# Performance work log

Measured on AMD Instinct MI355X. Metric: run time of the kernel, lower is better.

## Reference

```python
import jax, jax.numpy as jnp
import numpy as np

EMBED = 768
HEADS = 12
HEAD_DIM = EMBED // HEADS
HIDDEN = 4 * EMBED
EPS = 1e-5


def _layernorm(x, g, b):
    mu = jnp.mean(x, axis=-1, keepdims=True)
    var = jnp.var(x, axis=-1, keepdims=True)
    return (x - mu) * jax.lax.rsqrt(var + EPS) * g + b


def setup_inputs() -> dict:
    key = jax.random.key(0)
    ks = jax.random.split(key, 12)
    s_e = 1.0 / np.sqrt(EMBED)
    s_h = 1.0 / np.sqrt(HIDDEN)
    return {
        "x": jax.random.normal(ks[0], (2, 2048, EMBED), dtype=jnp.float32),
        "ln1_g": jnp.ones((EMBED,), jnp.float32),
        "ln1_b": jnp.zeros((EMBED,), jnp.float32),
        "qkv_w": jax.random.uniform(ks[1], (EMBED, 3 * EMBED), jnp.float32, -s_e, s_e),
        "qkv_b": jax.random.uniform(ks[2], (3 * EMBED,), jnp.float32, -s_e, s_e),
        "proj_w": jax.random.uniform(ks[3], (EMBED, EMBED), jnp.float32, -s_e, s_e),
        "proj_b": jax.random.uniform(ks[4], (EMBED,), jnp.float32, -s_e, s_e),
        "ln2_g": jnp.ones((EMBED,), jnp.float32),
        "ln2_b": jnp.zeros((EMBED,), jnp.float32),
        "fc1_w": jax.random.uniform(ks[5], (EMBED, HIDDEN), jnp.float32, -s_e, s_e),
        "fc1_b": jax.random.uniform(ks[6], (HIDDEN,), jnp.float32, -s_e, s_e),
        "fc2_w": jax.random.uniform(ks[7], (HIDDEN, EMBED), jnp.float32, -s_h, s_h),
        "fc2_b": jax.random.uniform(ks[8], (EMBED,), jnp.float32, -s_h, s_h),
    }


def reference(x, ln1_g, ln1_b, qkv_w, qkv_b, proj_w, proj_b,
              ln2_g, ln2_b, fc1_w, fc1_b, fc2_w, fc2_b):
    B, L, C = x.shape
    scale = HEAD_DIM ** -0.5

    # --- attention sublayer (pre-LN) ---
    h = _layernorm(x, ln1_g, ln1_b)
    qkv = h @ qkv_w + qkv_b                       # [B, L, 3C]
    qkv = qkv.reshape(B, L, 3, HEADS, HEAD_DIM)
    q = jnp.transpose(qkv[:, :, 0], (0, 2, 1, 3))  # [B, H, L, D]
    k = jnp.transpose(qkv[:, :, 1], (0, 2, 1, 3))
    v = jnp.transpose(qkv[:, :, 2], (0, 2, 1, 3))
    attn = jnp.einsum('bhqd,bhkd->bhqk', q, k) * scale  # [B, H, L, L]
    attn = jax.nn.softmax(attn, axis=-1)
    out = jnp.einsum('bhqk,bhkd->bhqd', attn, v)  # [B, H, L, D]
    out = jnp.transpose(out, (0, 2, 1, 3)).reshape(B, L, C)
    x = x + (out @ proj_w + proj_b)

    # --- FFN sublayer (pre-LN) ---
    h = _layernorm(x, ln2_g, ln2_b)
    h = jax.nn.gelu(h @ fc1_w + fc1_b, approximate=False)
    x = x + (h @ fc2_w + fc2_b)
    return x
```

## Files before the change

kernel.cpp:

```cpp
#include <hip/hip_runtime.h>
#include <hip/hip_bf16.h>
#include <math.h>

#define EMBED   768
#define NHEADS  12
#define HD      64
#define HIDDEN  3072
#define SEQ     2048
#define BATCH   2
#define ROWS    (BATCH*SEQ)

#define QSCALE  0.1803368801111204f

typedef __bf16 bf16_t;
typedef __attribute__((ext_vector_type(8))) __bf16 bf16x8;
typedef __attribute__((ext_vector_type(4))) float f32x4;

static __device__ __forceinline__ f32x4 mfma16(bf16x8 a, bf16x8 b, f32x4 c) {
  return __builtin_amdgcn_mfma_f32_16x16x32_bf16(a, b, c, 0, 0, 0);
}

#if __has_builtin(__builtin_amdgcn_exp2f)
static __device__ __forceinline__ float fast_exp2(float x) {
  return __builtin_amdgcn_exp2f(x);
}
#else
static __device__ __forceinline__ float fast_exp2(float x) { return exp2f(x); }
#endif

#if __has_builtin(__builtin_amdgcn_rcpf)
static __device__ __forceinline__ float fast_rcp(float x) {
  return __builtin_amdgcn_rcpf(x);
}
#else
static __device__ __forceinline__ float fast_rcp(float x) { return 1.0f / x; }
#endif

typedef __attribute__((address_space(1))) const void gas_void;
typedef __attribute__((address_space(3))) void las_void;
static __device__ __forceinline__ void gll16(const void* g, void* l) {
  __builtin_amdgcn_global_load_lds((gas_void*)g, (las_void*)l, 16, 0, 0);
}

__global__ __launch_bounds__(256) void prep_kernel(
    const float* __restrict__ w0, bf16_t* __restrict__ o0,
    const float* __restrict__ w1, bf16_t* __restrict__ o1,
    const float* __restrict__ w2, bf16_t* __restrict__ o2,
    const float* __restrict__ w3, bf16_t* __restrict__ o3,
    const float* __restrict__ x,  const float* __restrict__ g,
    const float* __restrict__ bt, bf16_t* __restrict__ lnout)
{
  __shared__ float tile[32][33];
  __shared__ float red[8];
  int lin = blockIdx.x;
  if (lin < 6912) {
    const float* in; bf16_t* out; int R, C, bx, by;
    if (lin < 1728)      { in = w0; out = o0; R = 768;  C = 2304; bx = lin % 72; by = lin / 72; }
    else if (lin < 2304) { in = w1; out = o1; R = 768;  C = 768;  lin -= 1728; bx = lin % 24; by = lin / 24; }
    else if (lin < 4608) { in = w2; out = o2; R = 768;  C = 3072; lin -= 2304; bx = lin % 96; by = lin / 96; }
    else                 { in = w3; out = o3; R = 3072; C = 768;  lin -= 4608; bx = lin % 24; by = lin / 24; }
    int c0 = bx * 32, r0 = by * 32;
    int tx = threadIdx.x & 31, ty = threadIdx.x >> 5;
    #pragma unroll
    for (int p = 0; p < 4; ++p) {
      int r = ty + p * 8;
      tile[r][tx] = in[(size_t)(r0 + r) * C + c0 + tx];
    }
    __syncthreads();
    #pragma unroll
    for (int p = 0; p < 4; ++p) {
      int cc = ty + p * 8;
      out[(size_t)(c0 + cc) * R + r0 + tx] = (bf16_t)tile[tx][cc];
    }
    return;
  }
  int row = lin - 6912;
  int tid = threadIdx.x;
  const float* xr = x + (size_t)row * EMBED;
  float v0 = xr[tid], v1 = xr[tid + 256], v2 = xr[tid + 512];
  float s  = v0 + v1 + v2;
  float s2 = v0*v0 + v1*v1 + v2*v2;
  #pragma unroll
  for (int o = 32; o >= 1; o >>= 1) {
    s  += __shfl_xor(s,  o, 64);
    s2 += __shfl_xor(s2, o, 64);
  }
  int wave = tid >> 6, lane = tid & 63;
  if (lane == 0) { red[wave] = s; red[wave + 4] = s2; }
  __syncthreads();
  s  = red[0] + red[1] + red[2] + red[3];
  s2 = red[4] + red[5] + red[6] + red[7];
  float mu  = s * (1.0f / EMBED);
  float var = s2 * (1.0f / EMBED) - mu * mu;
  float rs  = rsqrtf(var + 1e-5f);
  bf16_t* orow = lnout + (size_t)row * EMBED;
  orow[tid]       = (bf16_t)((v0 - mu) * rs * g[tid]       + bt[tid]);
  orow[tid + 256] = (bf16_t)((v1 - mu) * rs * g[tid + 256] + bt[tid + 256]);
  orow[tid + 512] = (bf16_t)((v2 - mu) * rs * g[tid + 512] + bt[tid + 512]);
}

__global__ __launch_bounds__(256) void ln_kernel(
    const float* __restrict__ x, const float* __restrict__ g,
    const float* __restrict__ bt, bf16_t* __restrict__ out)
{
  int row = blockIdx.x;
  int tid = threadIdx.x;
  const float* xr = x + (size_t)row * EMBED;
  float v0 = xr[tid], v1 = xr[tid + 256], v2 = xr[tid + 512];
  float s  = v0 + v1 + v2;
  float s2 = v0*v0 + v1*v1 + v2*v2;
  #pragma unroll
  for (int o = 32; o >= 1; o >>= 1) {
    s  += __shfl_xor(s,  o, 64);
    s2 += __shfl_xor(s2, o, 64);
  }
  __shared__ float red[8];
  int wave = tid >> 6, lane = tid & 63;
  if (lane == 0) { red[wave] = s; red[wave + 4] = s2; }
  __syncthreads();
  s  = red[0] + red[1] + red[2] + red[3];
  s2 = red[4] + red[5] + red[6] + red[7];
  float mu  = s * (1.0f / EMBED);
  float var = s2 * (1.0f / EMBED) - mu * mu;
  float rs  = rsqrtf(var + 1e-5f);
  bf16_t* orow = out + (size_t)row * EMBED;
  orow[tid]       = (bf16_t)((v0 - mu) * rs * g[tid]       + bt[tid]);
  orow[tid + 256] = (bf16_t)((v1 - mu) * rs * g[tid + 256] + bt[tid + 256]);
  orow[tid + 512] = (bf16_t)((v2 - mu) * rs * g[tid + 512] + bt[tid + 512]);
}

template<int MODE, int BN>
__global__ __launch_bounds__(256) void gemm_kernel(
    const bf16_t* __restrict__ A, const bf16_t* __restrict__ WT,
    const float* __restrict__ bias, const float* __restrict__ res,
    void* __restrict__ outp, bf16_t* __restrict__ vt, int N, int K)
{
  constexpr int JT = BN / 32;
  __shared__ bf16_t As[128 * 64];
  __shared__ bf16_t Bs[BN * 64];
  int tid = threadIdx.x;
  int lane = tid & 63, wave = tid >> 6;
  int l15 = lane & 15, quad = lane >> 4;
  int wm = wave >> 1, wn = wave & 1;

  int Nn = N / BN;
  int lin = blockIdx.x;
  int khalf = 0, k_lo = 0, k_hi = K;
  if (MODE == 4) { khalf = lin & 1; lin >>= 1; k_lo = khalf * (K / 2); k_hi = k_lo + K / 2; }
  int bm = (lin & 7) + 8 * ((lin >> 3) / Nn);
  int bn = (lin >> 3) % Nn;
  int m0 = bm * 128, n0 = bn * BN;

  f32x4 acc[4][JT];
  #pragma unroll
  for (int i = 0; i < 4; ++i)
    #pragma unroll
    for (int j = 0; j < JT; ++j)
      acc[i][j] = (f32x4){0.f, 0.f, 0.f, 0.f};

  int grow = lane >> 3;
  int gcol = ((lane & 7) ^ grow) * 8;
  const bf16_t* abase = A  + (size_t)(m0 + wave * 32 + grow) * K + gcol;
  const bf16_t* bbase = WT + (size_t)(n0 + wave * (BN / 4) + grow) * K + gcol;
  int swk = l15 & 7;

  for (int k0 = k_lo; k0 < k_hi; k0 += 64) {
    #pragma unroll
    for (int a = 0; a < 4; ++a)
      gll16(abase + (size_t)a * 8 * K + k0, &As[(wave * 32 + a * 8) * 64]);
    #pragma unroll
    for (int a = 0; a < BN / 32; ++a)
      gll16(bbase + (size_t)a * 8 * K + k0, &Bs[(wave * (BN / 4) + a * 8) * 64]);
    __syncthreads();

    #pragma unroll
    for (int g = 0; g < 2; ++g) {
      bf16x8 af[4], bfr[JT];
      #pragma unroll
      for (int i = 0; i < 4; ++i)
        af[i] = *(const bf16x8*)
            &As[(wm * 64 + i * 16 + l15) * 64 + (((g * 4 + quad) ^ swk) * 8)];
      #pragma unroll
      for (int j = 0; j < JT; ++j)
        bfr[j] = *(const bf16x8*)
            &Bs[(wn * (BN / 2) + j * 16 + l15) * 64 + (((g * 4 + quad) ^ swk) * 8)];
      #pragma unroll
      for (int i = 0; i < 4; ++i)
        #pragma unroll
        for (int j = 0; j < JT; ++j)
          acc[i][j] = mfma16(af[i], bfr[j], acc[i][j]);
    }
    __syncthreads();
  }

  #pragma unroll
  for (int i = 0; i < 4; ++i) {
    int mbase = m0 + wm * 64 + i * 16 + quad * 4;
    #pragma unroll
    for (int j = 0; j < JT; ++j) {
      int n = n0 + wn * (BN / 2) + j * 16 + l15;
      float bn_ = (MODE == 4 && khalf != 0) ? 0.f : bias[n];
      if (MODE == 3 && n >= 1536) {
        int dcol = n - 1536;
        int hh = dcol >> 6, dd = dcol & 63;
        int bsel = mbase >> 11, l = mbase & 2047;
        union { bf16_t b4[4]; uint2 u; } pk;
        #pragma unroll
        for (int r = 0; r < 4; ++r)
          pk.b4[r] = (bf16_t)(acc[i][j][r] + bn_);
        *(uint2*)&vt[(((size_t)bsel * NHEADS + hh) * HD + dd) * SEQ + l] = pk.u;
        continue;
      }
      #pragma unroll
      for (int r = 0; r < 4; ++r) {
        size_t idx = (size_t)(mbase + r) * N + n;
        float v = acc[i][j][r] + bn_;
        if (MODE == 1) {
          float e = fast_exp2(fminf(v * (2.3020807f + 0.10293776f * v * v), 120.f));
          v = v * e * fast_rcp(e + 1.0f);
        }
        if (MODE == 3 && n < 768) v *= QSCALE;
        if (MODE == 2) {
          v += res[idx];
          ((float*)outp)[idx] = v;
        } else if (MODE == 4) {
          atomicAdd((float*)outp + idx, v);
        } else {
          ((bf16_t*)outp)[idx] = (bf16_t)v;
        }
      }
    }
  }
}

__global__ __launch_bounds__(256, 2) void attn_kernel(
    const bf16_t* __restrict__ qkv, const bf16_t* __restrict__ vt,
    bf16_t* __restrict__ attnout)
{
  __attribute__((aligned(16))) __shared__ bf16_t smem[4 * 8192 + 4 * 2 * 640];
  __shared__ float dsumf[4][128];

  int qt = blockIdx.x, h = blockIdx.y, b = blockIdx.z;
  int tid = threadIdx.x;
  int wave = tid >> 6, lane = tid & 63;
  int l15 = lane & 15, quad = lane >> 4;
  int q0 = qt * 128;
  int bh = b * NHEADS + h;

  bf16_t* wbase = smem + wave * 8192;
  bf16_t* pt0   = smem + 32768 + wave * 1280;

  bf16x8 bq[8][2];
  #pragma unroll
  for (int qi = 0; qi < 8; ++qi) {
    const bf16_t* qrow = qkv + (size_t)(b * SEQ + q0 + qi * 16 + l15) * 2304
                             + h * HD + quad * 8;
    bq[qi][0] = *(const bf16x8*)qrow;
    bq[qi][1] = *(const bf16x8*)(qrow + 32);
  }
  __asm__ volatile("s_waitcnt vmcnt(0)" ::: "memory");

  f32x4 accO[8][4];
  #pragma unroll
  for (int qi = 0; qi < 8; ++qi)
    #pragma unroll
    for (int t2 = 0; t2 < 4; ++t2)
      accO[qi][t2] = (f32x4){0.f, 0.f, 0.f, 0.f};
  float lpart[8] = {};

  int krow_l = lane >> 3;
  int kchunk = ((lane & 7) ^ krow_l) * 8;
  const bf16_t* ksrc0 = qkv + (size_t)(b * SEQ + wave * 32 + krow_l) * 2304
                            + 768 + h * HD + kchunk;
  int vrow_l = lane >> 2;
  int vchunk = ((lane & 3) ^ (vrow_l & 3)) * 8;
  const bf16_t* vsrc0 = vt + ((size_t)bh * HD + vrow_l) * SEQ + wave * 32 + vchunk;

  constexpr int NIT = SEQ / 128;

  {
    bf16_t* kb = wbase;
    bf16_t* vb = wbase + 2048;
    #pragma unroll
    for (int p = 0; p < 4; ++p) {
      gll16(ksrc0 + (size_t)(p * 8) * 2304, kb + p * 512);
      gll16(vsrc0 + (size_t)(p * 16) * SEQ, vb + p * 512);
    }
  }

  int cb = 0;
  for (int it = 0; it < NIT; ++it) {
    {
      int kvn = ((it + 1) & (NIT - 1)) * 128;
      const bf16_t* ks = ksrc0 + (size_t)kvn * 2304;
      const bf16_t* vs = vsrc0 + kvn;
      bf16_t* kb = wbase + (cb ^ 1) * 4096;
      bf16_t* vb = kb + 2048;
      #pragma unroll
      for (int p = 0; p < 4; ++p) {
        gll16(ks + (size_t)(p * 8) * 2304, kb + p * 512);
        gll16(vs + (size_t)(p * 16) * SEQ, vb + p * 512);
      }
    }
    __asm__ volatile("s_waitcnt vmcnt(8)" ::: "memory");

    const bf16_t* kb = wbase + cb * 4096;
    const bf16_t* vb = kb + 2048;

    bf16x8 ak[2][2];
    #pragma unroll
    for (int t = 0; t < 2; ++t)
      #pragma unroll
      for (int f = 0; f < 2; ++f)
        ak[t][f] = *(const bf16x8*)
            &kb[(t * 16 + l15) * 64 + (((f * 4 + quad) ^ (l15 & 7)) * 8)];

    bf16x8 bv[4];
    #pragma unroll
    for (int t2 = 0; t2 < 4; ++t2)
      bv[t2] = *(const bf16x8*)
          &vb[(t2 * 16 + l15) * 32 + ((quad ^ (l15 & 3)) * 8)];

    #pragma unroll
    for (int qi = 0; qi < 8; ++qi) {
      bf16_t* pt = pt0 + (qi & 1) * 640;
      #pragma unroll
      for (int t = 0; t < 2; ++t) {
        f32x4 s = (f32x4){0.f, 0.f, 0.f, 0.f};
        s = mfma16(ak[t][0], bq[qi][0], s);
        s = mfma16(ak[t][1], bq[qi][1], s);
        union { bf16_t b4[4]; uint2 u; } pk;
        float ls = 0.f;
        #pragma unroll
        for (int r = 0; r < 4; ++r) {
          float pv = fast_exp2(s[r]);
          ls += pv;
          pk.b4[r] = (bf16_t)pv;
        }
        lpart[qi] += ls;
        *(uint2*)&pt[l15 * 40 + t * 16 + quad * 4] = pk.u;
      }
      bf16x8 ap = *(const bf16x8*)&pt[l15 * 40 + quad * 8];
      #pragma unroll
      for (int t2 = 0; t2 < 4; ++t2)
        accO[qi][t2] = mfma16(ap, bv[t2], accO[qi][t2]);
    }
    cb ^= 1;
  }

  #pragma unroll
  for (int qi = 0; qi < 8; ++qi) {
    float l = lpart[qi];
    l += __shfl_xor(l, 16, 64);
    l += __shfl_xor(l, 32, 64);
    if (quad == 0) dsumf[wave][qi * 16 + l15] = l;
  }
  __syncthreads();

  float* slabf = (float*)smem;
  int rq = lane >> 3;
  int d0 = (lane & 7) * 8;

  for (int pass = 0; pass < 4; ++pass) {
    #pragma unroll
    for (int qi2 = 0; qi2 < 2; ++qi2) {
      int qi = pass * 2 + qi2;
      #pragma unroll
      for (int t2 = 0; t2 < 4; ++t2)
        #pragma unroll
        for (int r = 0; r < 4; ++r)
          slabf[wave * 2048 + (qi2 * 16 + quad * 4 + r) * 64 + t2 * 16 + l15]
              = accO[qi][t2][r];
    }
    __syncthreads();
    int q_loc = wave * 8 + rq;
    f32x4 o0 = (f32x4){0.f,0.f,0.f,0.f}, o1 = (f32x4){0.f,0.f,0.f,0.f};
    #pragma unroll
    for (int sw = 0; sw < 4; ++sw) {
      o0 += *(const f32x4*)&slabf[sw * 2048 + q_loc * 64 + d0];
      o1 += *(const f32x4*)&slabf[sw * 2048 + q_loc * 64 + d0 + 4];
    }
    int q_abs = pass * 32 + q_loc;
    float den = dsumf[0][q_abs] + dsumf[1][q_abs] + dsumf[2][q_abs] + dsumf[3][q_abs];
    float inv = 1.0f / den;
    bf16_t ob[8];
    #pragma unroll
    for (int j = 0; j < 4; ++j) {
      ob[j]     = (bf16_t)(o0[j] * inv);
      ob[j + 4] = (bf16_t)(o1[j] * inv);
    }
    *(uint4*)&attnout[(size_t)(b * SEQ + q0 + q_abs) * EMBED + h * HD + d0]
        = *(const uint4*)ob;
    if (pass < 3) __syncthreads();
  }
}

extern "C" void kernel_launch(void* const* d_in, const int* in_sizes, int n_in,
                              void* d_out, int out_size, void* d_ws, size_t ws_size,
                              hipStream_t stream) {
  (void)in_sizes; (void)n_in; (void)out_size; (void)ws_size;
  const float* x      = (const float*)d_in[0];
  const float* ln1_g  = (const float*)d_in[1];
  const float* ln1_b  = (const float*)d_in[2];
  const float* qkv_w  = (const float*)d_in[3];
  const float* qkv_b  = (const float*)d_in[4];
  const float* proj_w = (const float*)d_in[5];
  const float* proj_b = (const float*)d_in[6];
  const float* ln2_g  = (const float*)d_in[7];
  const float* ln2_b  = (const float*)d_in[8];
  const float* fc1_w  = (const float*)d_in[9];
  const float* fc1_b  = (const float*)d_in[10];
  const float* fc2_w  = (const float*)d_in[11];
  const float* fc2_b  = (const float*)d_in[12];
  float* out = (float*)d_out;

  char* p = (char*)d_ws;
  bf16_t* wqkvT  = (bf16_t*)p; p += (size_t)2304 * 768 * 2;
  bf16_t* wprojT = (bf16_t*)p; p += (size_t)768 * 768 * 2;
  bf16_t* wfc1T  = (bf16_t*)p; p += (size_t)3072 * 768 * 2;
  bf16_t* wfc2T  = (bf16_t*)p; p += (size_t)768 * 3072 * 2;
  bf16_t* hbuf   = (bf16_t*)p; p += (size_t)ROWS * 768 * 2;
  bf16_t* qkv    = (bf16_t*)p;
  bf16_t* hid    = (bf16_t*)p; p += (size_t)ROWS * 3072 * 2;
  bf16_t* vt     = (bf16_t*)p; p += (size_t)BATCH * NHEADS * HD * SEQ * 2;
  bf16_t* attno  = (bf16_t*)p; p += (size_t)ROWS * 768 * 2;

  prep_kernel<<<6912 + ROWS, 256, 0, stream>>>(
      qkv_w, wqkvT, proj_w, wprojT, fc1_w, wfc1T, fc2_w, wfc2T,
      x, ln1_g, ln1_b, hbuf);

  gemm_kernel<3,128><<<32 * (2304/128), 256, 0, stream>>>(
      hbuf, wqkvT, qkv_b, nullptr, qkv, vt, 2304, 768);
  attn_kernel<<<dim3(SEQ/128, NHEADS, BATCH), 256, 0, stream>>>(qkv, vt, attno);
  gemm_kernel<2,64><<<32 * (768/64), 256, 0, stream>>>(
      attno, wprojT, proj_b, x, out, nullptr, 768, 768);

  ln_kernel<<<ROWS, 256, 0, stream>>>(out, ln2_g, ln2_b, hbuf);
  gemm_kernel<1,128><<<32 * (3072/128), 256, 0, stream>>>(
      hbuf, wfc1T, fc1_b, nullptr, hid, nullptr, 3072, 768);
  gemm_kernel<4,64><<<2 * 32 * (768/64), 256, 0, stream>>>(
      hid, wfc2T, fc2_b, nullptr, out, nullptr, 768, 3072);
}
```

Measured before the change: 269.6 us.

## Shrink attention query tile to 64 and feed P to PV MFMA from registers

```diff
diff --git a/kernel.cpp b/kernel.cpp
--- a/kernel.cpp
+++ b/kernel.cpp
@@ -14,13 +14,37 @@
 
 typedef __bf16 bf16_t;
 typedef __attribute__((ext_vector_type(8))) __bf16 bf16x8;
+typedef __attribute__((ext_vector_type(4))) __bf16 bf16x4;
+typedef __attribute__((ext_vector_type(4))) short s16x4;
 typedef __attribute__((ext_vector_type(4))) float f32x4;
 
 static __device__ __forceinline__ f32x4 mfma16(bf16x8 a, bf16x8 b, f32x4 c) {
   return __builtin_amdgcn_mfma_f32_16x16x32_bf16(a, b, c, 0, 0, 0);
 }
 
-#if __has_builtin(__builtin_amdgcn_exp2f)
+static __device__ __forceinline__ f32x4 mfma16x16(bf16x4 a, bf16x4 b, f32x4 c) {
+#if defined(__HIP_DEVICE_COMPILE__)
+# if __has_builtin(__builtin_amdgcn_mfma_f32_16x16x16bf16_1k)
+  s16x4 ai, bi;
+  __builtin_memcpy(&ai, &a, 8);
+  __builtin_memcpy(&bi, &b, 8);
+  return __builtin_amdgcn_mfma_f32_16x16x16bf16_1k(ai, bi, c, 0, 0, 0);
+# elif __has_builtin(__builtin_amdgcn_mfma_f32_16x16x16_bf16)
+  return __builtin_amdgcn_mfma_f32_16x16x16_bf16(a, b, c, 0, 0, 0);
+# else
+  bf16x8 a8 = {a[0], a[1], a[2], a[3],
+               (bf16_t)0.f, (bf16_t)0.f, (bf16_t)0.f, (bf16_t)0.f};
+  bf16x8 b8 = {b[0], b[1], b[2], b[3],
+               (bf16_t)0.f, (bf16_t)0.f, (bf16_t)0.f, (bf16_t)0.f};
+  return mfma16(a8, b8, c);
+# endif
+#else
+  (void)a; (void)b;
+  return c;
+#endif
+}
+
+#if defined(__HIP_DEVICE_COMPILE__) && __has_builtin(__builtin_amdgcn_exp2f)
 static __device__ __forceinline__ float fast_exp2(float x) {
   return __builtin_amdgcn_exp2f(x);
 }
@@ -28,7 +52,7 @@
 static __device__ __forceinline__ float fast_exp2(float x) { return exp2f(x); }
 #endif
 
-#if __has_builtin(__builtin_amdgcn_rcpf)
+#if defined(__HIP_DEVICE_COMPILE__) && __has_builtin(__builtin_amdgcn_rcpf)
 static __device__ __forceinline__ float fast_rcp(float x) {
   return __builtin_amdgcn_rcpf(x);
 }
@@ -233,26 +257,25 @@
   }
 }
 
-__global__ __launch_bounds__(256, 2) void attn_kernel(
+__global__ __launch_bounds__(256, 3) void attn_kernel(
     const bf16_t* __restrict__ qkv, const bf16_t* __restrict__ vt,
     bf16_t* __restrict__ attnout)
 {
-  __attribute__((aligned(16))) __shared__ bf16_t smem[4 * 8192 + 4 * 2 * 640];
-  __shared__ float dsumf[4][128];
+  __attribute__((aligned(16))) __shared__ bf16_t smem[4 * 4096];
+  __shared__ float dsumf[4][64];
 
   int qt = blockIdx.x, h = blockIdx.y, b = blockIdx.z;
   int tid = threadIdx.x;
   int wave = tid >> 6, lane = tid & 63;
   int l15 = lane & 15, quad = lane >> 4;
-  int q0 = qt * 128;
+  int q0 = qt * 64;
   int bh = b * NHEADS + h;
 
-  bf16_t* wbase = smem + wave * 8192;
-  bf16_t* pt0   = smem + 32768 + wave * 1280;
-
-  bf16x8 bq[8][2];
-  #pragma unroll
-  for (int qi = 0; qi < 8; ++qi) {
+  bf16_t* wbase = smem + wave * 4096;
+
+  bf16x8 bq[4][2];
+  #pragma unroll
+  for (int qi = 0; qi < 4; ++qi) {
     const bf16_t* qrow = qkv + (size_t)(b * SEQ + q0 + qi * 16 + l15) * 2304
                              + h * HD + quad * 8;
     bq[qi][0] = *(const bf16x8*)qrow;
@@ -260,96 +283,87 @@
   }
   __asm__ volatile("s_waitcnt vmcnt(0)" ::: "memory");
 
-  f32x4 accO[8][4];
-  #pragma unroll
-  for (int qi = 0; qi < 8; ++qi)
+  f32x4 accO[4][4];
+  #pragma unroll
+  for (int qi = 0; qi < 4; ++qi)
     #pragma unroll
     for (int t2 = 0; t2 < 4; ++t2)
       accO[qi][t2] = (f32x4){0.f, 0.f, 0.f, 0.f};
-  float lpart[8] = {};
+  float lpart[4] = {};
 
   int krow_l = lane >> 3;
   int kchunk = ((lane & 7) ^ krow_l) * 8;
-  const bf16_t* ksrc0 = qkv + (size_t)(b * SEQ + wave * 32 + krow_l) * 2304
+  const bf16_t* ksrc0 = qkv + (size_t)(b * SEQ + wave * 16 + krow_l) * 2304
                             + 768 + h * HD + kchunk;
-  int vrow_l = lane >> 2;
-  int vchunk = ((lane & 3) ^ (vrow_l & 3)) * 8;
-  const bf16_t* vsrc0 = vt + ((size_t)bh * HD + vrow_l) * SEQ + wave * 32 + vchunk;
-
-  constexpr int NIT = SEQ / 128;
+  int vrow_l = lane >> 1;
+  int vchunk = (lane & 1) * 8;
+  const bf16_t* vsrc0 = vt + ((size_t)bh * HD + vrow_l) * SEQ + wave * 16 + vchunk;
+
+  constexpr int NIT = SEQ / 64;
 
   {
     bf16_t* kb = wbase;
-    bf16_t* vb = wbase + 2048;
-    #pragma unroll
-    for (int p = 0; p < 4; ++p) {
+    bf16_t* vb = wbase + 1024;
+    #pragma unroll
+    for (int p = 0; p < 2; ++p) {
       gll16(ksrc0 + (size_t)(p * 8) * 2304, kb + p * 512);
-      gll16(vsrc0 + (size_t)(p * 16) * SEQ, vb + p * 512);
+      gll16(vsrc0 + (size_t)(p * 32) * SEQ, vb + p * 512);
     }
   }
 
   int cb = 0;
   for (int it = 0; it < NIT; ++it) {
     {
-      int kvn = ((it + 1) & (NIT - 1)) * 128;
+      int kvn = ((it + 1) & (NIT - 1)) * 64;
       const bf16_t* ks = ksrc0 + (size_t)kvn * 2304;
       const bf16_t* vs = vsrc0 + kvn;
-      bf16_t* kb = wbase + (cb ^ 1) * 4096;
-      bf16_t* vb = kb + 2048;
-      #pragma unroll
-      for (int p = 0; p < 4; ++p) {
+      bf16_t* kb = wbase + (cb ^ 1) * 2048;
+      bf16_t* vb = kb + 1024;
+      #pragma unroll
+      for (int p = 0; p < 2; ++p) {
         gll16(ks + (size_t)(p * 8) * 2304, kb + p * 512);
-        gll16(vs + (size_t)(p * 16) * SEQ, vb + p * 512);
+        gll16(vs + (size_t)(p * 32) * SEQ, vb + p * 512);
       }
     }
-    __asm__ volatile("s_waitcnt vmcnt(8)" ::: "memory");
-
-    const bf16_t* kb = wbase + cb * 4096;
-    const bf16_t* vb = kb + 2048;
-
-    bf16x8 ak[2][2];
-    #pragma unroll
-    for (int t = 0; t < 2; ++t)
-      #pragma unroll
-      for (int f = 0; f < 2; ++f)
-        ak[t][f] = *(const bf16x8*)
-            &kb[(t * 16 + l15) * 64 + (((f * 4 + quad) ^ (l15 & 7)) * 8)];
-
-    bf16x8 bv[4];
+    __asm__ volatile("s_waitcnt vmcnt(4)" ::: "memory");
+
+    const bf16_t* kb = wbase + cb * 2048;
+    const bf16_t* vb = kb + 1024;
+
+    bf16x8 ak[2];
+    #pragma unroll
+    for (int f = 0; f < 2; ++f)
+      ak[f] = *(const bf16x8*)
+          &kb[l15 * 64 + (((f * 4 + quad) ^ (l15 & 7)) * 8)];
+
+    bf16x4 bv[4];
     #pragma unroll
     for (int t2 = 0; t2 < 4; ++t2)
-      bv[t2] = *(const bf16x8*)
-          &vb[(t2 * 16 + l15) * 32 + ((quad ^ (l15 & 3)) * 8)];
-
-    #pragma unroll
-    for (int qi = 0; qi < 8; ++qi) {
-      bf16_t* pt = pt0 + (qi & 1) * 640;
-      #pragma unroll
-      for (int t = 0; t < 2; ++t) {
-        f32x4 s = (f32x4){0.f, 0.f, 0.f, 0.f};
-        s = mfma16(ak[t][0], bq[qi][0], s);
-        s = mfma16(ak[t][1], bq[qi][1], s);
-        union { bf16_t b4[4]; uint2 u; } pk;
-        float ls = 0.f;
-        #pragma unroll
-        for (int r = 0; r < 4; ++r) {
-          float pv = fast_exp2(s[r]);
-          ls += pv;
-          pk.b4[r] = (bf16_t)pv;
-        }
-        lpart[qi] += ls;
-        *(uint2*)&pt[l15 * 40 + t * 16 + quad * 4] = pk.u;
+      bv[t2] = *(const bf16x4*)&vb[(t2 * 16 + l15) * 16 + quad * 4];
+
+    #pragma unroll
+    for (int qi = 0; qi < 4; ++qi) {
+      f32x4 s = (f32x4){0.f, 0.f, 0.f, 0.f};
+      s = mfma16(ak[0], bq[qi][0], s);
+      s = mfma16(ak[1], bq[qi][1], s);
+      bf16x4 ap;
+      float ls = 0.f;
+      #pragma unroll
+      for (int r = 0; r < 4; ++r) {
+        float pv = fast_exp2(s[r]);
+        ls += pv;
+        ap[r] = (bf16_t)pv;
       }
-      bf16x8 ap = *(const bf16x8*)&pt[l15 * 40 + quad * 8];
+      lpart[qi] += ls;
       #pragma unroll
       for (int t2 = 0; t2 < 4; ++t2)
-        accO[qi][t2] = mfma16(ap, bv[t2], accO[qi][t2]);
+        accO[qi][t2] = mfma16x16(ap, bv[t2], accO[qi][t2]);
     }
     cb ^= 1;
   }
 
   #pragma unroll
-  for (int qi = 0; qi < 8; ++qi) {
+  for (int qi = 0; qi < 4; ++qi) {
     float l = lpart[qi];
     l += __shfl_xor(l, 16, 64);
     l += __shfl_xor(l, 32, 64);
@@ -358,10 +372,8 @@
   __syncthreads();
 
   float* slabf = (float*)smem;
-  int rq = lane >> 3;
-  int d0 = (lane & 7) * 8;
-
-  for (int pass = 0; pass < 4; ++pass) {
+
+  for (int pass = 0; pass < 2; ++pass) {
     #pragma unroll
     for (int qi2 = 0; qi2 < 2; ++qi2) {
       int qi = pass * 2 + qi2;
@@ -373,14 +385,15 @@
               = accO[qi][t2][r];
     }
     __syncthreads();
-    int q_loc = wave * 8 + rq;
+    int row = tid >> 3;
+    int d0 = (tid & 7) * 8;
     f32x4 o0 = (f32x4){0.f,0.f,0.f,0.f}, o1 = (f32x4){0.f,0.f,0.f,0.f};
     #pragma unroll
     for (int sw = 0; sw < 4; ++sw) {
-      o0 += *(const f32x4*)&slabf[sw * 2048 + q_loc * 64 + d0];
-      o1 += *(const f32x4*)&slabf[sw * 2048 + q_loc * 64 + d0 + 4];
-    }
-    int q_abs = pass * 32 + q_loc;
+      o0 += *(const f32x4*)&slabf[sw * 2048 + row * 64 + d0];
+      o1 += *(const f32x4*)&slabf[sw * 2048 + row * 64 + d0 + 4];
+    }
+    int q_abs = pass * 32 + row;
     float den = dsumf[0][q_abs] + dsumf[1][q_abs] + dsumf[2][q_abs] + dsumf[3][q_abs];
     float inv = 1.0f / den;
     bf16_t ob[8];
@@ -391,7 +404,7 @@
     }
     *(uint4*)&attnout[(size_t)(b * SEQ + q0 + q_abs) * EMBED + h * HD + d0]
         = *(const uint4*)ob;
-    if (pass < 3) __syncthreads();
+    if (pass == 0) __syncthreads();
   }
 }
 
@@ -431,7 +444,7 @@
 
   gemm_kernel<3,128><<<32 * (2304/128), 256, 0, stream>>>(
       hbuf, wqkvT, qkv_b, nullptr, qkv, vt, 2304, 768);
-  attn_kernel<<<dim3(SEQ/128, NHEADS, BATCH), 256, 0, stream>>>(qkv, vt, attno);
+  attn_kernel<<<dim3(SEQ/64, NHEADS, BATCH), 256, 0, stream>>>(qkv, vt, attno);
   gemm_kernel<2,64><<<32 * (768/64), 256, 0, stream>>>(
       attno, wprojT, proj_b, x, out, nullptr, 768, 768);
 
```

After: 265.0 us. No clear change (-1.7%).
